# Optimization experiments

Hardware: AMD Instinct MI355X
Metric: run time of the kernel (lower is better)

Reference implementation:

```python
import jax, jax.numpy as jnp
import numpy as np

E, TOPK, D, F, FS = 16, 4, 2560, 1664, 3328
B, S = 1, 2048


def setup_inputs() -> dict:
    key = jax.random.key(0)
    ks = jax.random.split(key, 8)
    sc = lambda *sh: 1.0 / np.sqrt(sh[-2] if len(sh) > 1 else 1.0)
    return {
        "hidden_states": jax.random.normal(ks[0], (B, S, D), jnp.float32),
        "router_weight": jax.random.normal(ks[1], (E, D), jnp.float32) * (1.0 / np.sqrt(D)),
        "w_gate": jax.random.normal(ks[2], (E, D, F), jnp.float32) * (1.0 / np.sqrt(D)),
        "w_up": jax.random.normal(ks[3], (E, D, F), jnp.float32) * (1.0 / np.sqrt(D)),
        "w_down": jax.random.normal(ks[4], (E, F, D), jnp.float32) * (1.0 / np.sqrt(F)),
        "sw_gate": jax.random.normal(ks[5], (D, FS), jnp.float32) * (1.0 / np.sqrt(D)),
        "sw_up": jax.random.normal(ks[6], (D, FS), jnp.float32) * (1.0 / np.sqrt(D)),
        "sw_down": jax.random.normal(ks[7], (FS, D), jnp.float32) * (1.0 / np.sqrt(FS)),
    }


def reference(hidden_states, router_weight, w_gate, w_up, w_down, sw_gate, sw_up, sw_down):
    b, s, d = hidden_states.shape
    x = hidden_states.reshape(-1, d)  # [T, D]
    T = x.shape[0]

    # Router: linear -> softmax -> top-k -> renormalize (vLLM FusedMoE default)
    logits = x @ router_weight.T                      # [T, E]
    probs = jax.nn.softmax(logits, axis=-1)
    topk_w, topk_idx = jax.lax.top_k(probs, TOPK)     # [T, K]
    topk_w = topk_w / jnp.sum(topk_w, axis=-1, keepdims=True)
    combine = jnp.zeros((T, E), x.dtype).at[jnp.arange(T)[:, None], topk_idx].add(topk_w)  # [T, E]

    # Expert SiLU-gated MLPs (dense-dispatch reference for grouped GEMM)
    g = jnp.einsum('td,edf->tef', x, w_gate)          # [T, E, F]
    u = jnp.einsum('td,edf->tef', x, w_up)
    h = jax.nn.silu(g) * u
    y = jnp.einsum('tef,efd->ted', h, w_down)         # [T, E, D]
    sparse_out = jnp.einsum('ted,te->td', y, combine)

    # Shared expert: LlamaMLP with silu gate, no bias
    shared_out = (jax.nn.silu(x @ sw_gate) * (x @ sw_up)) @ sw_down

    return (sparse_out + shared_out).reshape(b, s, d)
```

## Files before the change

### kernel.cpp

```cpp
#include <hip/hip_runtime.h>
#include <hip/hip_bf16.h>
#include <stdint.h>

#define E_N 16
#define TOPK 4
#define DD 2560
#define FF 1664
#define FSS 3328
#define TT 2048

#define BK 32

typedef __attribute__((ext_vector_type(8))) __bf16 bf16x8;
typedef __attribute__((ext_vector_type(4))) float f32x4;

__device__ __forceinline__ unsigned short f2bf(float f) {
  return __builtin_bit_cast(unsigned short, (__bf16)f);
}
__device__ __forceinline__ unsigned int pk2(float a, float b) {
  return (unsigned int)f2bf(a) | ((unsigned int)f2bf(b) << 16);
}

#define GLOAD16(g, l)                                                          \
  __builtin_amdgcn_global_load_lds(                                            \
      (const __attribute__((address_space(1))) void*)(g),                      \
      (__attribute__((address_space(3))) void*)(l), 16, 0, 0)

#define SBAR() __builtin_amdgcn_s_barrier()
#define SCHED0() __builtin_amdgcn_sched_barrier(0)
#define VMW(N) asm volatile("s_waitcnt vmcnt(" #N ")" ::: "memory")

__device__ __forceinline__ void swz_block(int& bm, int& bn, int& bz) {
  int gx = gridDim.x, gy = gridDim.y;
  int nwg = gx * gy * gridDim.z;
  int flat = blockIdx.x + gx * (blockIdx.y + gy * blockIdx.z);
  if ((nwg & 7) == 0) flat = (flat & 7) * (nwg >> 3) + (flat >> 3);
  bm = flat % gx;
  int rest = flat / gx;
  bn = rest % gy;
  bz = rest / gy;
}

__global__ __launch_bounds__(256) void cvt_bf16_kernel(const float* __restrict__ in,
                                                       unsigned short* __restrict__ out) {
  size_t i = ((size_t)blockIdx.x * 256 + threadIdx.x) * 4;
  float4 v = *reinterpret_cast<const float4*>(in + i);
  ushort4 o;
  o.x = f2bf(v.x); o.y = f2bf(v.y); o.z = f2bf(v.z); o.w = f2bf(v.w);
  *reinterpret_cast<ushort4*>(out + i) = o;
}

__global__ __launch_bounds__(256) void tcvt_kernel(const float* __restrict__ in,
                                                   unsigned short* __restrict__ out,
                                                   int K, int N) {
  __shared__ float lds[64 * 65];
  int z = blockIdx.z;
  in += (size_t)z * K * N;
  out += (size_t)z * K * N;
  int k0 = blockIdx.x * 64, n0 = blockIdx.y * 64;
  int t = threadIdx.x;
#pragma unroll
  for (int j = 0; j < 4; ++j) {
    int idx = j * 256 + t;
    int r = idx >> 4, c = (idx & 15) * 4;
    float4 v = *reinterpret_cast<const float4*>(in + (size_t)(k0 + r) * N + n0 + c);
    lds[r * 65 + c] = v.x;
    lds[r * 65 + c + 1] = v.y;
    lds[r * 65 + c + 2] = v.z;
    lds[r * 65 + c + 3] = v.w;
  }
  __syncthreads();
#pragma unroll
  for (int j = 0; j < 2; ++j) {
    int idx = j * 256 + t;
    int n = idx >> 3, kg = (idx & 7) * 8;
    float a0 = lds[(kg + 0) * 65 + n], a1 = lds[(kg + 1) * 65 + n];
    float a2 = lds[(kg + 2) * 65 + n], a3 = lds[(kg + 3) * 65 + n];
    float a4 = lds[(kg + 4) * 65 + n], a5 = lds[(kg + 5) * 65 + n];
    float a6 = lds[(kg + 6) * 65 + n], a7 = lds[(kg + 7) * 65 + n];
    uint4 o{pk2(a0, a1), pk2(a2, a3), pk2(a4, a5), pk2(a6, a7)};
    *reinterpret_cast<uint4*>(out + (size_t)(n0 + n) * K + k0 + kg) = o;
  }
}

__global__ __launch_bounds__(256) void router_kernel(const float* __restrict__ x,
                                                     const float* __restrict__ rw,
                                                     int* __restrict__ cnt,
                                                     int* __restrict__ list,
                                                     float* __restrict__ tw) {
  int t = blockIdx.x;
  const float* xr = x + (size_t)t * DD;
  __shared__ float logits[E_N];
  int lane = threadIdx.x & 63, wid = threadIdx.x >> 6;
  for (int ee = 0; ee < 4; ++ee) {
    int e = wid * 4 + ee;
    const float* wr = rw + (size_t)e * DD;
    float p = 0.f;
    for (int d = lane; d < DD; d += 64) p += xr[d] * wr[d];
#pragma unroll
    for (int off = 32; off > 0; off >>= 1) p += __shfl_down(p, off);
    if (lane == 0) logits[e] = p;
  }
  __syncthreads();
  if (threadIdx.x == 0) {
    float mx = -1e30f;
    for (int e = 0; e < E_N; ++e) mx = fmaxf(mx, logits[e]);
    float pe[E_N];
    for (int e = 0; e < E_N; ++e) pe[e] = __expf(logits[e] - mx);
    int idx[TOPK]; float val[TOPK]; float s4 = 0.f;
    unsigned used = 0;
    for (int k = 0; k < TOPK; ++k) {
      int bi = 0; float bv = -1.f;
      for (int e = 0; e < E_N; ++e)
        if (!((used >> e) & 1) && pe[e] > bv) { bv = pe[e]; bi = e; }
      used |= 1u << bi; idx[k] = bi; val[k] = bv; s4 += bv;
    }
    float inv = 1.f / s4;
    for (int k = 0; k < TOPK; ++k) {
      int e2 = idx[k];
      int pos = atomicAdd(&cnt[e2], 1);
      list[e2 * TT + pos] = t * 4 + k;
      tw[t * 4 + k] = val[k] * inv;
    }
  }
}

__global__ __launch_bounds__(512, 2) void gu_kernel(
    const unsigned short* __restrict__ Xb,
    const unsigned short* __restrict__ WgT,
    const unsigned short* __restrict__ WuT,
    unsigned short* __restrict__ H,
    const int* __restrict__ list, const int* __restrict__ cnt,
    int Ktot, int Ntot, int Mfixed) {
  int bm, bn, e;
  swz_block(bm, bn, e);
  int M = cnt ? cnt[e] : Mfixed;
  int m0 = bm * 256;
  if (m0 >= M) return;
  int n0 = bn * 128;
  const unsigned short* Bg0 = WgT + (size_t)e * Ktot * Ntot;
  const unsigned short* Bu0 = WuT + (size_t)e * Ktot * Ntot;
  const int* lst = list ? (list + e * TT) : nullptr;

  __shared__ __align__(16) unsigned short lds[4][16384];

  int tid = threadIdx.x, lane = tid & 63, w = tid >> 6;
  int wm = w >> 1, wn = w & 1;

  const unsigned short* sp[4];
  {
    int rh = tid >> 2, c = tid & 3;
    int cs = (c ^ ((rh >> 1) & 3)) * 8;
    int a0 = min(m0 + rh, M - 1), a1 = min(m0 + 128 + rh, M - 1);
    int t0 = lst ? (lst[a0] >> 2) : a0;
    int t1 = lst ? (lst[a1] >> 2) : a1;
    sp[0] = Xb + (size_t)t0 * Ktot + cs;
    sp[1] = Xb + (size_t)t1 * Ktot + cs;
    sp[2] = Bg0 + (size_t)(n0 + rh) * Ktot + cs;
    sp[3] = Bu0 + (size_t)(n0 + rh) * Ktot + cs;
  }

  auto issue = [&](int kt, int buf) {
    int koff = kt * BK;
    unsigned short* d = &lds[buf][0];
#pragma unroll
    for (int j = 0; j < 4; ++j)
      GLOAD16(sp[j] + koff, d + j * 4096 + tid * 8);
  };

  int cg = lane >> 4;
  int aoff[4], goff[4];
#pragma unroll
  for (int mf = 0; mf < 4; ++mf) {
    int r = wm * 64 + mf * 16 + (lane & 15);
    aoff[mf] = r * 32 + ((cg ^ ((r >> 1) & 3)) * 8);
  }
#pragma unroll
  for (int nf = 0; nf < 4; ++nf) {
    int rb = wn * 64 + nf * 16 + (lane & 15);
    goff[nf] = 8192 + rb * 32 + ((cg ^ ((rb >> 1) & 3)) * 8);
  }

  f32x4 accG[4][4] = {};
  f32x4 accU[4][4] = {};

  auto compute = [&](int buf) {
    const unsigned short* L = &lds[buf][0];
    bf16x8 a[4], g[4], u[4];
#pragma unroll
    for (int mf = 0; mf < 4; ++mf)
      a[mf] = __builtin_bit_cast(bf16x8, *reinterpret_cast<const uint4*>(L + aoff[mf]));
#pragma unroll
    for (int nf = 0; nf < 4; ++nf) {
      g[nf] = __builtin_bit_cast(bf16x8, *reinterpret_cast<const uint4*>(L + goff[nf]));
      u[nf] = __builtin_bit_cast(bf16x8, *reinterpret_cast<const uint4*>(L + goff[nf] + 4096));
    }
    __builtin_amdgcn_s_setprio(1);
#pragma unroll
    for (int mf = 0; mf < 4; ++mf)
#pragma unroll
      for (int nf = 0; nf < 4; ++nf) {
        accG[mf][nf] = __builtin_amdgcn_mfma_f32_16x16x32_bf16(a[mf], g[nf], accG[mf][nf], 0, 0, 0);
        accU[mf][nf] = __builtin_amdgcn_mfma_f32_16x16x32_bf16(a[mf], u[nf], accU[mf][nf], 0, 0, 0);
      }
    __builtin_amdgcn_s_setprio(0);
  };

  int nk = Ktot / BK;
  issue(0, 0);
  issue(1, 1);
  issue(2, 2);
  for (int kt = 0; kt < nk; ++kt) {
    int rem = nk - 1 - kt;
    if (rem >= 3) { issue(kt + 3, (kt + 3) & 3); VMW(12); }
    else if (rem == 2) { VMW(8); }
    else if (rem == 1) { VMW(4); }
    else { VMW(0); }
    SCHED0();
    SBAR(); SCHED0();
    compute(kt & 3);
    SCHED0();
    SBAR(); SCHED0();
  }

#pragma unroll
  for (int mf = 0; mf < 4; ++mf) {
#pragma unroll
    for (int q = 0; q < 4; ++q) {
      int lr = wm * 64 + mf * 16 + (lane >> 4) * 4 + q;
      int grow = m0 + lr;
      if (grow < M) {
        int code = lst ? lst[grow] : grow;
        unsigned short* Hp = H + (size_t)code * Ntot + n0 + wn * 64 + (lane & 15);
#pragma unroll
        for (int nf = 0; nf < 4; ++nf) {
          float gg = accG[mf][nf][q], uu = accU[mf][nf][q];
          Hp[nf * 16] = f2bf((gg / (1.f + __expf(-gg))) * uu);
        }
      }
    }
  }
}

__global__ __launch_bounds__(512, 2) void dn_kernel(
    const unsigned short* __restrict__ Hb,
    const unsigned short* __restrict__ WT,
    float* __restrict__ Y,
    const int* __restrict__ list, const int* __restrict__ cnt,
    const float* __restrict__ tw, int Ktot, int Ntot, int Mfixed) {
  int bm, bn, e;
  swz_block(bm, bn, e);
  int M = cnt ? cnt[e] : Mfixed;
  int m0 = bm * 128;
  if (m0 >= M) return;
  int n0 = bn * 256;
  const unsigned short* B0 = WT + (size_t)e * Ktot * Ntot;
  const int* lst = list ? (list + e * TT) : nullptr;

  __shared__ __align__(16) unsigned short lds[4][12288];

  int tid = threadIdx.x, lane = tid & 63, w = tid >> 6;
  int wm = w >> 2, wn = w & 3;

  const unsigned short* sp[3];
  {
    int rh = tid >> 2, c = tid & 3;
    int cs = (c ^ ((rh >> 1) & 3)) * 8;
    int a0 = min(m0 + rh, M - 1);
    int code0 = lst ? lst[a0] : a0;
    sp[0] = Hb + (size_t)code0 * Ktot + cs;
    sp[1] = B0 + (size_t)(n0 + rh) * Ktot + cs;
    sp[2] = B0 + (size_t)(n0 + 128 + rh) * Ktot + cs;
  }

  auto issue = [&](int kt, int buf) {
    int koff = kt * BK;
    unsigned short* d = &lds[buf][0];
#pragma unroll
    for (int j = 0; j < 3; ++j)
      GLOAD16(sp[j] + koff, d + j * 4096 + tid * 8);
  };

  int cg = lane >> 4;
  int aoff[4], boff[4];
#pragma unroll
  for (int mf = 0; mf < 4; ++mf) {
    int r = wm * 64 + mf * 16 + (lane & 15);
    aoff[mf] = r * 32 + ((cg ^ ((r >> 1) & 3)) * 8);
  }
#pragma unroll
  for (int nf = 0; nf < 4; ++nf) {
    int rb = wn * 64 + nf * 16 + (lane & 15);
    boff[nf] = 4096 + rb * 32 + ((cg ^ ((rb >> 1) & 3)) * 8);
  }

  f32x4 acc[4][4] = {};

  auto compute = [&](int buf) {
    const unsigned short* L = &lds[buf][0];
    bf16x8 a[4], b[4];
#pragma unroll
    for (int mf = 0; mf < 4; ++mf)
      a[mf] = __builtin_bit_cast(bf16x8, *reinterpret_cast<const uint4*>(L + aoff[mf]));
#pragma unroll
    for (int nf = 0; nf < 4; ++nf)
      b[nf] = __builtin_bit_cast(bf16x8, *reinterpret_cast<const uint4*>(L + boff[nf]));
    __builtin_amdgcn_s_setprio(1);
#pragma unroll
    for (int mf = 0; mf < 4; ++mf)
#pragma unroll
      for (int nf = 0; nf < 4; ++nf)
        acc[mf][nf] = __builtin_amdgcn_mfma_f32_16x16x32_bf16(a[mf], b[nf], acc[mf][nf], 0, 0, 0);
    __builtin_amdgcn_s_setprio(0);
  };

  int nk = Ktot / BK;
  issue(0, 0);
  issue(1, 1);
  issue(2, 2);
  for (int kt = 0; kt < nk; ++kt) {
    int rem = nk - 1 - kt;
    if (rem >= 3) { issue(kt + 3, (kt + 3) & 3); VMW(9); }
    else if (rem == 2) { VMW(6); }
    else if (rem == 1) { VMW(3); }
    else { VMW(0); }
    SCHED0();
    SBAR(); SCHED0();
    compute(kt & 3);
    SCHED0();
    SBAR(); SCHED0();
  }

#pragma unroll
  for (int mf = 0; mf < 4; ++mf) {
#pragma unroll
    for (int q = 0; q < 4; ++q) {
      int lr = wm * 64 + mf * 16 + (lane >> 4) * 4 + q;
      int grow = m0 + lr;
      if (grow < M) {
        int code = lst ? lst[grow] : grow;
        float scale = tw ? tw[code] : 1.f;
        float* Yp = Y + (size_t)code * Ntot + n0 + wn * 64 + (lane & 15);
#pragma unroll
        for (int nf = 0; nf < 4; ++nf) Yp[nf * 16] = acc[mf][nf][q] * scale;
      }
    }
  }
}

__global__ __launch_bounds__(256) void combine_kernel(const float* __restrict__ Y,
                                                      const float* __restrict__ Ys,
                                                      float* __restrict__ out) {
  size_t i = ((size_t)blockIdx.x * 256 + threadIdx.x) * 4;
  size_t t = i / DD;
  int d = (int)(i % DD);
  float4 a = *reinterpret_cast<const float4*>(Ys + i);
#pragma unroll
  for (int k = 0; k < 4; ++k) {
    float4 v = *reinterpret_cast<const float4*>(Y + (t * 4 + k) * (size_t)DD + d);
    a.x += v.x; a.y += v.y; a.z += v.z; a.w += v.w;
  }
  *reinterpret_cast<float4*>(out + i) = a;
}

extern "C" void kernel_launch(void* const* d_in, const int* in_sizes, int n_in,
                              void* d_out, int out_size, void* d_ws, size_t ws_size,
                              hipStream_t stream) {
  const float* x  = (const float*)d_in[0];
  const float* rw = (const float*)d_in[1];
  const float* wg = (const float*)d_in[2];
  const float* wu = (const float*)d_in[3];
  const float* wd = (const float*)d_in[4];
  const float* sg = (const float*)d_in[5];
  const float* su = (const float*)d_in[6];
  const float* sd = (const float*)d_in[7];
  float* out = (float*)d_out;

  char* ws = (char*)d_ws;
  size_t off = 0;
  auto alloc = [&](size_t bytes) {
    off = (off + 255) & ~(size_t)255;
    void* p = ws + off;
    off += bytes;
    return p;
  };
  unsigned short* W1 = (unsigned short*)alloc((size_t)E_N * FF * DD * 2);
  unsigned short* W2 = (unsigned short*)alloc((size_t)E_N * FF * DD * 2);
  unsigned short* W3 = (unsigned short*)alloc((size_t)FSS * DD * 2);
  unsigned short* W4 = (unsigned short*)alloc((size_t)FSS * DD * 2);
  unsigned short* Xb = (unsigned short*)alloc((size_t)TT * DD * 2);
  unsigned short* Hx = (unsigned short*)alloc((size_t)4 * TT * FF * 2);
  unsigned short* Hs = (unsigned short*)alloc((size_t)TT * FSS * 2);
  float* Y  = (float*)alloc((size_t)4 * TT * DD * 4);
  float* Ys = (float*)alloc((size_t)TT * DD * 4);
  float* tw = (float*)alloc((size_t)4 * TT * 4);
  int* cnt  = (int*)alloc(E_N * 4);
  int* list = (int*)alloc((size_t)E_N * TT * 4);
  (void)ws_size; (void)in_sizes; (void)n_in; (void)out_size;

  hipMemsetAsync(cnt, 0, E_N * 4, stream);
  cvt_bf16_kernel<<<TT * DD / 4 / 256, 256, 0, stream>>>(x, Xb);
  router_kernel<<<TT, 256, 0, stream>>>(x, rw, cnt, list, tw);

  tcvt_kernel<<<dim3(DD / 64, FF / 64, E_N), 256, 0, stream>>>(wg, W1, DD, FF);
  tcvt_kernel<<<dim3(DD / 64, FF / 64, E_N), 256, 0, stream>>>(wu, W2, DD, FF);
  tcvt_kernel<<<dim3(DD / 64, FSS / 64, 1), 256, 0, stream>>>(sg, W3, DD, FSS);
  tcvt_kernel<<<dim3(DD / 64, FSS / 64, 1), 256, 0, stream>>>(su, W4, DD, FSS);

  gu_kernel<<<dim3(TT * 4 / 256, FF / 128, E_N), 512, 0, stream>>>(
      Xb, W1, W2, Hx, list, cnt, DD, FF, 0);
  gu_kernel<<<dim3(TT / 256, FSS / 128, 1), 512, 0, stream>>>(
      Xb, W3, W4, Hs, nullptr, nullptr, DD, FSS, TT);

  tcvt_kernel<<<dim3(FF / 64, DD / 64, E_N), 256, 0, stream>>>(wd, W1, FF, DD);
  tcvt_kernel<<<dim3(FSS / 64, DD / 64, 1), 256, 0, stream>>>(sd, W2, FSS, DD);

  dn_kernel<<<dim3(TT * 4 / 128, DD / 256, E_N), 512, 0, stream>>>(
      Hx, W1, Y, list, cnt, tw, FF, DD, 0);
  dn_kernel<<<dim3(TT / 128, DD / 256, 1), 512, 0, stream>>>(
      Hs, W2, Ys, nullptr, nullptr, nullptr, FSS, DD, TT);

  combine_kernel<<<TT * DD / 4 / 256, 256, 0, stream>>>(Y, Ys, out);
}
```

Baseline: 1.159 ms.

## Fuse fp32 weight transpose-convert into grouped GEMM B-tile loads

Removes the separate transpose-and-convert kernels that wrote bf16 copies of every expert and shared weight. The GEMM kernels now read fp32 weights straight from global memory into registers, pack them to bf16 and store them transposed into swizzled LDS. They double-buffer A through global-to-LDS loads and B through registers. Tiles shrink to 128x128 with 256 threads, which raises occupancy but doubles fp32 weight traffic per byte used and reloads weights once for each M tile.

```diff
diff --git a/kernel.cpp b/kernel.cpp
--- a/kernel.cpp
+++ b/kernel.cpp
@@ -9,8 +9,6 @@
 #define FSS 3328
 #define TT 2048
 
-#define BK 32
-
 typedef __attribute__((ext_vector_type(8))) __bf16 bf16x8;
 typedef __attribute__((ext_vector_type(4))) float f32x4;
 
@@ -29,6 +27,7 @@
 #define SBAR() __builtin_amdgcn_s_barrier()
 #define SCHED0() __builtin_amdgcn_sched_barrier(0)
 #define VMW(N) asm volatile("s_waitcnt vmcnt(" #N ")" ::: "memory")
+#define LGKM0() asm volatile("s_waitcnt lgkmcnt(0)" ::: "memory")
 
 __device__ __forceinline__ void swz_block(int& bm, int& bn, int& bz) {
   int gx = gridDim.x, gy = gridDim.y;
@@ -48,39 +47,6 @@
   ushort4 o;
   o.x = f2bf(v.x); o.y = f2bf(v.y); o.z = f2bf(v.z); o.w = f2bf(v.w);
   *reinterpret_cast<ushort4*>(out + i) = o;
-}
-
-__global__ __launch_bounds__(256) void tcvt_kernel(const float* __restrict__ in,
-                                                   unsigned short* __restrict__ out,
-                                                   int K, int N) {
-  __shared__ float lds[64 * 65];
-  int z = blockIdx.z;
-  in += (size_t)z * K * N;
-  out += (size_t)z * K * N;
-  int k0 = blockIdx.x * 64, n0 = blockIdx.y * 64;
-  int t = threadIdx.x;
-#pragma unroll
-  for (int j = 0; j < 4; ++j) {
-    int idx = j * 256 + t;
-    int r = idx >> 4, c = (idx & 15) * 4;
-    float4 v = *reinterpret_cast<const float4*>(in + (size_t)(k0 + r) * N + n0 + c);
-    lds[r * 65 + c] = v.x;
-    lds[r * 65 + c + 1] = v.y;
-    lds[r * 65 + c + 2] = v.z;
-    lds[r * 65 + c + 3] = v.w;
-  }
-  __syncthreads();
-#pragma unroll
-  for (int j = 0; j < 2; ++j) {
-    int idx = j * 256 + t;
-    int n = idx >> 3, kg = (idx & 7) * 8;
-    float a0 = lds[(kg + 0) * 65 + n], a1 = lds[(kg + 1) * 65 + n];
-    float a2 = lds[(kg + 2) * 65 + n], a3 = lds[(kg + 3) * 65 + n];
-    float a4 = lds[(kg + 4) * 65 + n], a5 = lds[(kg + 5) * 65 + n];
-    float a6 = lds[(kg + 6) * 65 + n], a7 = lds[(kg + 7) * 65 + n];
-    uint4 o{pk2(a0, a1), pk2(a2, a3), pk2(a4, a5), pk2(a6, a7)};
-    *reinterpret_cast<uint4*>(out + (size_t)(n0 + n) * K + k0 + kg) = o;
-  }
 }
 
 __global__ __launch_bounds__(256) void router_kernel(const float* __restrict__ x,
@@ -125,51 +91,52 @@
   }
 }
 
-__global__ __launch_bounds__(512, 2) void gu_kernel(
+__global__ __launch_bounds__(256, 2) void gu_kernel(
     const unsigned short* __restrict__ Xb,
-    const unsigned short* __restrict__ WgT,
-    const unsigned short* __restrict__ WuT,
+    const float* __restrict__ Wg,
+    const float* __restrict__ Wu,
     unsigned short* __restrict__ H,
     const int* __restrict__ list, const int* __restrict__ cnt,
     int Ktot, int Ntot, int Mfixed) {
   int bm, bn, e;
   swz_block(bm, bn, e);
   int M = cnt ? cnt[e] : Mfixed;
-  int m0 = bm * 256;
+  int m0 = bm * 128;
   if (m0 >= M) return;
   int n0 = bn * 128;
-  const unsigned short* Bg0 = WgT + (size_t)e * Ktot * Ntot;
-  const unsigned short* Bu0 = WuT + (size_t)e * Ktot * Ntot;
+  const float* G0 = Wg + (size_t)e * Ktot * Ntot;
+  const float* U0 = Wu + (size_t)e * Ktot * Ntot;
   const int* lst = list ? (list + e * TT) : nullptr;
 
-  __shared__ __align__(16) unsigned short lds[4][16384];
+  __shared__ __align__(16) unsigned short sA[2][4096];
+  __shared__ __align__(16) unsigned short sG[2][4096];
+  __shared__ __align__(16) unsigned short sU[2][4096];
 
   int tid = threadIdx.x, lane = tid & 63, w = tid >> 6;
-  int wm = w >> 1, wn = w & 1;
-
-  const unsigned short* sp[4];
-  {
-    int rh = tid >> 2, c = tid & 3;
-    int cs = (c ^ ((rh >> 1) & 3)) * 8;
-    int a0 = min(m0 + rh, M - 1), a1 = min(m0 + 128 + rh, M - 1);
-    int t0 = lst ? (lst[a0] >> 2) : a0;
-    int t1 = lst ? (lst[a1] >> 2) : a1;
-    sp[0] = Xb + (size_t)t0 * Ktot + cs;
-    sp[1] = Xb + (size_t)t1 * Ktot + cs;
-    sp[2] = Bg0 + (size_t)(n0 + rh) * Ktot + cs;
-    sp[3] = Bu0 + (size_t)(n0 + rh) * Ktot + cs;
-  }
-
-  auto issue = [&](int kt, int buf) {
-    int koff = kt * BK;
-    unsigned short* d = &lds[buf][0];
-#pragma unroll
-    for (int j = 0; j < 4; ++j)
-      GLOAD16(sp[j] + koff, d + j * 4096 + tid * 8);
-  };
-
-  int cg = lane >> 4;
-  int aoff[4], goff[4];
+
+  const unsigned short* pA[2];
+#pragma unroll
+  for (int q = 0; q < 2; ++q) {
+    int row = q * 64 + (tid >> 2);
+    int cs = (tid & 3) ^ ((row >> 1) & 3);
+    int ar = min(m0 + row, M - 1);
+    int tok = lst ? (lst[ar] >> 2) : ar;
+    pA[q] = Xb + (size_t)tok * Ktot + cs * 8;
+  }
+
+  int kq = tid >> 5, nq = tid & 31;
+  const float* pG = G0 + (size_t)(kq * 4) * Ntot + n0 + nq * 4;
+  const float* pU = U0 + (size_t)(kq * 4) * Ntot + n0 + nq * 4;
+
+  int wB[4];
+#pragma unroll
+  for (int i = 0; i < 4; ++i) {
+    int r = nq * 4 + i;
+    wB[i] = r * 32 + (((kq >> 1) ^ ((r >> 1) & 3)) * 8) + ((kq & 1) * 4);
+  }
+
+  int wm = w >> 1, wn = w & 1, cg = lane >> 4;
+  int aoff[4], boff[4];
 #pragma unroll
   for (int mf = 0; mf < 4; ++mf) {
     int r = wm * 64 + mf * 16 + (lane & 15);
@@ -178,22 +145,42 @@
 #pragma unroll
   for (int nf = 0; nf < 4; ++nf) {
     int rb = wn * 64 + nf * 16 + (lane & 15);
-    goff[nf] = 8192 + rb * 32 + ((cg ^ ((rb >> 1) & 3)) * 8);
+    boff[nf] = rb * 32 + ((cg ^ ((rb >> 1) & 3)) * 8);
   }
 
   f32x4 accG[4][4] = {};
   f32x4 accU[4][4] = {};
-
-  auto compute = [&](int buf) {
-    const unsigned short* L = &lds[buf][0];
+  float4 rG[4], rU[4];
+
+  auto issueA = [&](int kt, int b) {
+    GLOAD16(pA[0] + kt * 32, &sA[b][tid * 8]);
+    GLOAD16(pA[1] + kt * 32, &sA[b][2048 + tid * 8]);
+  };
+  auto issueB = [&](int kt) {
+#pragma unroll
+    for (int j = 0; j < 4; ++j) {
+      rG[j] = *reinterpret_cast<const float4*>(pG + (size_t)(kt * 32 + j) * Ntot);
+      rU[j] = *reinterpret_cast<const float4*>(pU + (size_t)(kt * 32 + j) * Ntot);
+    }
+  };
+  auto writeB = [&](int b) {
+#pragma unroll
+    for (int i = 0; i < 4; ++i) {
+      uint2 vg{pk2(rG[0][i], rG[1][i]), pk2(rG[2][i], rG[3][i])};
+      uint2 vu{pk2(rU[0][i], rU[1][i]), pk2(rU[2][i], rU[3][i])};
+      *reinterpret_cast<uint2*>(&sG[b][wB[i]]) = vg;
+      *reinterpret_cast<uint2*>(&sU[b][wB[i]]) = vu;
+    }
+  };
+  auto compute = [&](int b) {
     bf16x8 a[4], g[4], u[4];
 #pragma unroll
     for (int mf = 0; mf < 4; ++mf)
-      a[mf] = __builtin_bit_cast(bf16x8, *reinterpret_cast<const uint4*>(L + aoff[mf]));
+      a[mf] = __builtin_bit_cast(bf16x8, *reinterpret_cast<const uint4*>(&sA[b][aoff[mf]]));
 #pragma unroll
     for (int nf = 0; nf < 4; ++nf) {
-      g[nf] = __builtin_bit_cast(bf16x8, *reinterpret_cast<const uint4*>(L + goff[nf]));
-      u[nf] = __builtin_bit_cast(bf16x8, *reinterpret_cast<const uint4*>(L + goff[nf] + 4096));
+      g[nf] = __builtin_bit_cast(bf16x8, *reinterpret_cast<const uint4*>(&sG[b][boff[nf]]));
+      u[nf] = __builtin_bit_cast(bf16x8, *reinterpret_cast<const uint4*>(&sU[b][boff[nf]]));
     }
     __builtin_amdgcn_s_setprio(1);
 #pragma unroll
@@ -206,21 +193,26 @@
     __builtin_amdgcn_s_setprio(0);
   };
 
-  int nk = Ktot / BK;
-  issue(0, 0);
-  issue(1, 1);
-  issue(2, 2);
+  int nk = Ktot / 32;
+  issueB(0);
+  SCHED0();
+  issueA(0, 0);
+  issueA(1, 1);
+  SCHED0();
   for (int kt = 0; kt < nk; ++kt) {
-    int rem = nk - 1 - kt;
-    if (rem >= 3) { issue(kt + 3, (kt + 3) & 3); VMW(12); }
-    else if (rem == 2) { VMW(8); }
-    else if (rem == 1) { VMW(4); }
-    else { VMW(0); }
+    int b = kt & 1;
+    if (kt == nk - 1) { VMW(0); } else { VMW(2); }
+    SCHED0();
+    writeB(b);
+    if (kt + 1 < nk) issueB(kt + 1);
+    SCHED0();
+    LGKM0();
     SCHED0();
     SBAR(); SCHED0();
-    compute(kt & 3);
+    compute(b);
     SCHED0();
     SBAR(); SCHED0();
+    if (kt + 2 < nk) { issueA(kt + 2, b); SCHED0(); }
   }
 
 #pragma unroll
@@ -242,9 +234,9 @@
   }
 }
 
-__global__ __launch_bounds__(512, 2) void dn_kernel(
+__global__ __launch_bounds__(256, 3) void dn_kernel(
     const unsigned short* __restrict__ Hb,
-    const unsigned short* __restrict__ WT,
+    const float* __restrict__ Wd,
     float* __restrict__ Y,
     const int* __restrict__ list, const int* __restrict__ cnt,
     const float* __restrict__ tw, int Ktot, int Ntot, int Mfixed) {
@@ -253,35 +245,36 @@
   int M = cnt ? cnt[e] : Mfixed;
   int m0 = bm * 128;
   if (m0 >= M) return;
-  int n0 = bn * 256;
-  const unsigned short* B0 = WT + (size_t)e * Ktot * Ntot;
+  int n0 = bn * 128;
+  const float* B0 = Wd + (size_t)e * Ktot * Ntot;
   const int* lst = list ? (list + e * TT) : nullptr;
 
-  __shared__ __align__(16) unsigned short lds[4][12288];
+  __shared__ __align__(16) unsigned short sA[2][4096];
+  __shared__ __align__(16) unsigned short sB[2][4096];
 
   int tid = threadIdx.x, lane = tid & 63, w = tid >> 6;
-  int wm = w >> 2, wn = w & 3;
-
-  const unsigned short* sp[3];
-  {
-    int rh = tid >> 2, c = tid & 3;
-    int cs = (c ^ ((rh >> 1) & 3)) * 8;
-    int a0 = min(m0 + rh, M - 1);
-    int code0 = lst ? lst[a0] : a0;
-    sp[0] = Hb + (size_t)code0 * Ktot + cs;
-    sp[1] = B0 + (size_t)(n0 + rh) * Ktot + cs;
-    sp[2] = B0 + (size_t)(n0 + 128 + rh) * Ktot + cs;
-  }
-
-  auto issue = [&](int kt, int buf) {
-    int koff = kt * BK;
-    unsigned short* d = &lds[buf][0];
-#pragma unroll
-    for (int j = 0; j < 3; ++j)
-      GLOAD16(sp[j] + koff, d + j * 4096 + tid * 8);
-  };
-
-  int cg = lane >> 4;
+
+  const unsigned short* pA[2];
+#pragma unroll
+  for (int q = 0; q < 2; ++q) {
+    int row = q * 64 + (tid >> 2);
+    int cs = (tid & 3) ^ ((row >> 1) & 3);
+    int ar = min(m0 + row, M - 1);
+    int code = lst ? lst[ar] : ar;
+    pA[q] = Hb + (size_t)code * Ktot + cs * 8;
+  }
+
+  int kq = tid >> 5, nq = tid & 31;
+  const float* pB = B0 + (size_t)(kq * 4) * Ntot + n0 + nq * 4;
+
+  int wB[4];
+#pragma unroll
+  for (int i = 0; i < 4; ++i) {
+    int r = nq * 4 + i;
+    wB[i] = r * 32 + (((kq >> 1) ^ ((r >> 1) & 3)) * 8) + ((kq & 1) * 4);
+  }
+
+  int wm = w >> 1, wn = w & 1, cg = lane >> 4;
   int aoff[4], boff[4];
 #pragma unroll
   for (int mf = 0; mf < 4; ++mf) {
@@ -291,44 +284,65 @@
 #pragma unroll
   for (int nf = 0; nf < 4; ++nf) {
     int rb = wn * 64 + nf * 16 + (lane & 15);
-    boff[nf] = 4096 + rb * 32 + ((cg ^ ((rb >> 1) & 3)) * 8);
+    boff[nf] = rb * 32 + ((cg ^ ((rb >> 1) & 3)) * 8);
   }
 
   f32x4 acc[4][4] = {};
-
-  auto compute = [&](int buf) {
-    const unsigned short* L = &lds[buf][0];
-    bf16x8 a[4], b[4];
+  float4 rB[4];
+
+  auto issueA = [&](int kt, int b) {
+    GLOAD16(pA[0] + kt * 32, &sA[b][tid * 8]);
+    GLOAD16(pA[1] + kt * 32, &sA[b][2048 + tid * 8]);
+  };
+  auto issueB = [&](int kt) {
+#pragma unroll
+    for (int j = 0; j < 4; ++j)
+      rB[j] = *reinterpret_cast<const float4*>(pB + (size_t)(kt * 32 + j) * Ntot);
+  };
+  auto writeB = [&](int b) {
+#pragma unroll
+    for (int i = 0; i < 4; ++i) {
+      uint2 vb{pk2(rB[0][i], rB[1][i]), pk2(rB[2][i], rB[3][i])};
+      *reinterpret_cast<uint2*>(&sB[b][wB[i]]) = vb;
+    }
+  };
+  auto compute = [&](int b) {
+    bf16x8 a[4], bb[4];
 #pragma unroll
     for (int mf = 0; mf < 4; ++mf)
-      a[mf] = __builtin_bit_cast(bf16x8, *reinterpret_cast<const uint4*>(L + aoff[mf]));
+      a[mf] = __builtin_bit_cast(bf16x8, *reinterpret_cast<const uint4*>(&sA[b][aoff[mf]]));
 #pragma unroll
     for (int nf = 0; nf < 4; ++nf)
-      b[nf] = __builtin_bit_cast(bf16x8, *reinterpret_cast<const uint4*>(L + boff[nf]));
+      bb[nf] = __builtin_bit_cast(bf16x8, *reinterpret_cast<const uint4*>(&sB[b][boff[nf]]));
     __builtin_amdgcn_s_setprio(1);
 #pragma unroll
     for (int mf = 0; mf < 4; ++mf)
 #pragma unroll
       for (int nf = 0; nf < 4; ++nf)
-        acc[mf][nf] = __builtin_amdgcn_mfma_f32_16x16x32_bf16(a[mf], b[nf], acc[mf][nf], 0, 0, 0);
+        acc[mf][nf] = __builtin_amdgcn_mfma_f32_16x16x32_bf16(a[mf], bb[nf], acc[mf][nf], 0, 0, 0);
     __builtin_amdgcn_s_setprio(0);
   };
 
-  int nk = Ktot / BK;
-  issue(0, 0);
-  issue(1, 1);
-  issue(2, 2);
+  int nk = Ktot / 32;
+  issueB(0);
+  SCHED0();
+  issueA(0, 0);
+  issueA(1, 1);
+  SCHED0();
   for (int kt = 0; kt < nk; ++kt) {
-    int rem = nk - 1 - kt;
-    if (rem >= 3) { issue(kt + 3, (kt + 3) & 3); VMW(9); }
-    else if (rem == 2) { VMW(6); }
-    else if (rem == 1) { VMW(3); }
-    else { VMW(0); }
+    int b = kt & 1;
+    if (kt == nk - 1) { VMW(0); } else { VMW(2); }
+    SCHED0();
+    writeB(b);
+    if (kt + 1 < nk) issueB(kt + 1);
+    SCHED0();
+    LGKM0();
     SCHED0();
     SBAR(); SCHED0();
-    compute(kt & 3);
+    compute(b);
     SCHED0();
     SBAR(); SCHED0();
+    if (kt + 2 < nk) { issueA(kt + 2, b); SCHED0(); }
   }
 
 #pragma unroll
@@ -384,10 +398,6 @@
     off += bytes;
     return p;
   };
-  unsigned short* W1 = (unsigned short*)alloc((size_t)E_N * FF * DD * 2);
-  unsigned short* W2 = (unsigned short*)alloc((size_t)E_N * FF * DD * 2);
-  unsigned short* W3 = (unsigned short*)alloc((size_t)FSS * DD * 2);
-  unsigned short* W4 = (unsigned short*)alloc((size_t)FSS * DD * 2);
   unsigned short* Xb = (unsigned short*)alloc((size_t)TT * DD * 2);
   unsigned short* Hx = (unsigned short*)alloc((size_t)4 * TT * FF * 2);
   unsigned short* Hs = (unsigned short*)alloc((size_t)TT * FSS * 2);
@@ -402,23 +412,14 @@
   cvt_bf16_kernel<<<TT * DD / 4 / 256, 256, 0, stream>>>(x, Xb);
   router_kernel<<<TT, 256, 0, stream>>>(x, rw, cnt, list, tw);
 
-  tcvt_kernel<<<dim3(DD / 64, FF / 64, E_N), 256, 0, stream>>>(wg, W1, DD, FF);
-  tcvt_kernel<<<dim3(DD / 64, FF / 64, E_N), 256, 0, stream>>>(wu, W2, DD, FF);
-  tcvt_kernel<<<dim3(DD / 64, FSS / 64, 1), 256, 0, stream>>>(sg, W3, DD, FSS);
-  tcvt_kernel<<<dim3(DD / 64, FSS / 64, 1), 256, 0, stream>>>(su, W4, DD, FSS);
-
-  gu_kernel<<<dim3(TT * 4 / 256, FF / 128, E_N), 512, 0, stream>>>(
-      Xb, W1, W2, Hx, list, cnt, DD, FF, 0);
-  gu_kernel<<<dim3(TT / 256, FSS / 128, 1), 512, 0, stream>>>(
-      Xb, W3, W4, Hs, nullptr, nullptr, DD, FSS, TT);
-
-  tcvt_kernel<<<dim3(FF / 64, DD / 64, E_N), 256, 0, stream>>>(wd, W1, FF, DD);
-  tcvt_kernel<<<dim3(FSS / 64, DD / 64, 1), 256, 0, stream>>>(sd, W2, FSS, DD);
-
-  dn_kernel<<<dim3(TT * 4 / 128, DD / 256, E_N), 512, 0, stream>>>(
-      Hx, W1, Y, list, cnt, tw, FF, DD, 0);
-  dn_kernel<<<dim3(TT / 128, DD / 256, 1), 512, 0, stream>>>(
-      Hs, W2, Ys, nullptr, nullptr, nullptr, FSS, DD, TT);
+  gu_kernel<<<dim3(TT * 4 / 128, FF / 128, E_N), 256, 0, stream>>>(
+      Xb, wg, wu, Hx, list, cnt, DD, FF, 0);
+  gu_kernel<<<dim3(TT / 128, FSS / 128, 1), 256, 0, stream>>>(
+      Xb, sg, su, Hs, nullptr, nullptr, DD, FSS, TT);
+  dn_kernel<<<dim3(TT * 4 / 128, DD / 128, E_N), 256, 0, stream>>>(
+      Hx, wd, Y, list, cnt, tw, FF, DD, 0);
+  dn_kernel<<<dim3(TT / 128, DD / 128, 1), 256, 0, stream>>>(
+      Hs, sd, Ys, nullptr, nullptr, nullptr, FSS, DD, TT);
 
   combine_kernel<<<TT * DD / 4 / 256, 256, 0, stream>>>(Y, Ys, out);
 }
```

New measurement: 1.184 ms. +2.2%, slower.

## Unify GEMMs into one 256x256-tile kernel and split SiLU into a separate pass

Applied to the files above, without the earlier changes.

Replaces the fused gate/up kernel and the down-projection kernel with one templated 256x256-tile bf16 MFMA GEMM. It drops the trailing barrier by issuing the next prefetch after the leading barrier into the buffer freed in the previous iteration. Gate and up projections now run as separate GEMMs writing bf16 intermediates, and a new elementwise kernel applies SiLU(g)*u in place. The larger down-projection tile and the single barrier are meant to improve reuse and cut sync cost. In exchange it adds an extra launch and a global write and read of the gate intermediate, plus padded, bounds-checked tiles because FF is not a multiple of 256.

```diff
diff --git a/kernel.cpp b/kernel.cpp
--- a/kernel.cpp
+++ b/kernel.cpp
@@ -16,6 +16,9 @@
 
 __device__ __forceinline__ unsigned short f2bf(float f) {
   return __builtin_bit_cast(unsigned short, (__bf16)f);
+}
+__device__ __forceinline__ float bf2f(unsigned short u) {
+  return __builtin_bit_cast(float, (unsigned int)u << 16);
 }
 __device__ __forceinline__ unsigned int pk2(float a, float b) {
   return (unsigned int)f2bf(a) | ((unsigned int)f2bf(b) << 16);
@@ -125,84 +128,84 @@
   }
 }
 
-__global__ __launch_bounds__(512, 2) void gu_kernel(
-    const unsigned short* __restrict__ Xb,
-    const unsigned short* __restrict__ WgT,
-    const unsigned short* __restrict__ WuT,
-    unsigned short* __restrict__ H,
+template <int MODE>
+__global__ __launch_bounds__(512, 2) void g1_kernel(
+    const unsigned short* __restrict__ Ab,
+    const unsigned short* __restrict__ WT,
+    void* __restrict__ Out,
     const int* __restrict__ list, const int* __restrict__ cnt,
+    const float* __restrict__ tw,
     int Ktot, int Ntot, int Mfixed) {
   int bm, bn, e;
   swz_block(bm, bn, e);
   int M = cnt ? cnt[e] : Mfixed;
   int m0 = bm * 256;
   if (m0 >= M) return;
-  int n0 = bn * 128;
-  const unsigned short* Bg0 = WgT + (size_t)e * Ktot * Ntot;
-  const unsigned short* Bu0 = WuT + (size_t)e * Ktot * Ntot;
+  int n0 = bn * 256;
+  const unsigned short* B0 = WT + (size_t)e * Ktot * Ntot;
   const int* lst = list ? (list + e * TT) : nullptr;
 
   __shared__ __align__(16) unsigned short lds[4][16384];
 
   int tid = threadIdx.x, lane = tid & 63, w = tid >> 6;
-  int wm = w >> 1, wn = w & 1;
-
-  const unsigned short* sp[4];
-  {
-    int rh = tid >> 2, c = tid & 3;
-    int cs = (c ^ ((rh >> 1) & 3)) * 8;
-    int a0 = min(m0 + rh, M - 1), a1 = min(m0 + 128 + rh, M - 1);
-    int t0 = lst ? (lst[a0] >> 2) : a0;
-    int t1 = lst ? (lst[a1] >> 2) : a1;
-    sp[0] = Xb + (size_t)t0 * Ktot + cs;
-    sp[1] = Xb + (size_t)t1 * Ktot + cs;
-    sp[2] = Bg0 + (size_t)(n0 + rh) * Ktot + cs;
-    sp[3] = Bu0 + (size_t)(n0 + rh) * Ktot + cs;
+  int wm = w >> 2, wn = w & 3;
+
+  const unsigned short* pA[2];
+  const unsigned short* pB[2];
+#pragma unroll
+  for (int j = 0; j < 2; ++j) {
+    int idx = j * 512 + tid;
+    int row = idx >> 2, c = idx & 3;
+    int cs = c ^ ((row >> 1) & 3);
+    int ar = min(m0 + row, M - 1);
+    int code = lst ? lst[ar] : ar;
+    int arow = (MODE == 0) ? (lst ? (code >> 2) : code) : code;
+    pA[j] = Ab + (size_t)arow * Ktot + cs * 8;
+    int br = min(n0 + row, Ntot - 1);
+    pB[j] = B0 + (size_t)br * Ktot + cs * 8;
   }
 
   auto issue = [&](int kt, int buf) {
     int koff = kt * BK;
     unsigned short* d = &lds[buf][0];
 #pragma unroll
-    for (int j = 0; j < 4; ++j)
-      GLOAD16(sp[j] + koff, d + j * 4096 + tid * 8);
+    for (int j = 0; j < 2; ++j)
+      GLOAD16(pA[j] + koff, d + (j * 512 + tid) * 8);
+#pragma unroll
+    for (int j = 0; j < 2; ++j)
+      GLOAD16(pB[j] + koff, d + 8192 + (j * 512 + tid) * 8);
   };
 
   int cg = lane >> 4;
-  int aoff[4], goff[4];
-#pragma unroll
-  for (int mf = 0; mf < 4; ++mf) {
-    int r = wm * 64 + mf * 16 + (lane & 15);
+  int aoff[8], boff[4];
+#pragma unroll
+  for (int mf = 0; mf < 8; ++mf) {
+    int r = wm * 128 + mf * 16 + (lane & 15);
     aoff[mf] = r * 32 + ((cg ^ ((r >> 1) & 3)) * 8);
   }
 #pragma unroll
   for (int nf = 0; nf < 4; ++nf) {
     int rb = wn * 64 + nf * 16 + (lane & 15);
-    goff[nf] = 8192 + rb * 32 + ((cg ^ ((rb >> 1) & 3)) * 8);
-  }
-
-  f32x4 accG[4][4] = {};
-  f32x4 accU[4][4] = {};
+    boff[nf] = 8192 + rb * 32 + ((cg ^ ((rb >> 1) & 3)) * 8);
+  }
+
+  f32x4 acc[8][4] = {};
 
   auto compute = [&](int buf) {
     const unsigned short* L = &lds[buf][0];
-    bf16x8 a[4], g[4], u[4];
-#pragma unroll
-    for (int mf = 0; mf < 4; ++mf)
+    bf16x8 a[8], b[4];
+#pragma unroll
+    for (int mf = 0; mf < 8; ++mf)
       a[mf] = __builtin_bit_cast(bf16x8, *reinterpret_cast<const uint4*>(L + aoff[mf]));
 #pragma unroll
-    for (int nf = 0; nf < 4; ++nf) {
-      g[nf] = __builtin_bit_cast(bf16x8, *reinterpret_cast<const uint4*>(L + goff[nf]));
-      u[nf] = __builtin_bit_cast(bf16x8, *reinterpret_cast<const uint4*>(L + goff[nf] + 4096));
-    }
+    for (int nf = 0; nf < 4; ++nf)
+      b[nf] = __builtin_bit_cast(bf16x8, *reinterpret_cast<const uint4*>(L + boff[nf]));
     __builtin_amdgcn_s_setprio(1);
 #pragma unroll
-    for (int mf = 0; mf < 4; ++mf)
-#pragma unroll
-      for (int nf = 0; nf < 4; ++nf) {
-        accG[mf][nf] = __builtin_amdgcn_mfma_f32_16x16x32_bf16(a[mf], g[nf], accG[mf][nf], 0, 0, 0);
-        accU[mf][nf] = __builtin_amdgcn_mfma_f32_16x16x32_bf16(a[mf], u[nf], accU[mf][nf], 0, 0, 0);
-      }
+    for (int mf = 0; mf < 8; ++mf)
+#pragma unroll
+      for (int nf = 0; nf < 4; ++nf)
+        acc[mf][nf] = __builtin_amdgcn_mfma_f32_16x16x32_bf16(a[mf], b[nf], acc[mf][nf], 0, 0, 0);
     __builtin_amdgcn_s_setprio(0);
   };
 
@@ -212,140 +215,62 @@
   issue(2, 2);
   for (int kt = 0; kt < nk; ++kt) {
     int rem = nk - 1 - kt;
-    if (rem >= 3) { issue(kt + 3, (kt + 3) & 3); VMW(12); }
-    else if (rem == 2) { VMW(8); }
+    if (rem >= 2) { VMW(8); }
     else if (rem == 1) { VMW(4); }
     else { VMW(0); }
     SCHED0();
     SBAR(); SCHED0();
+    if (rem >= 3) { issue(kt + 3, (kt + 3) & 3); SCHED0(); }
     compute(kt & 3);
     SCHED0();
-    SBAR(); SCHED0();
-  }
-
-#pragma unroll
-  for (int mf = 0; mf < 4; ++mf) {
+  }
+
+#pragma unroll
+  for (int mf = 0; mf < 8; ++mf) {
 #pragma unroll
     for (int q = 0; q < 4; ++q) {
-      int lr = wm * 64 + mf * 16 + (lane >> 4) * 4 + q;
+      int lr = wm * 128 + mf * 16 + (lane >> 4) * 4 + q;
       int grow = m0 + lr;
       if (grow < M) {
         int code = lst ? lst[grow] : grow;
-        unsigned short* Hp = H + (size_t)code * Ntot + n0 + wn * 64 + (lane & 15);
-#pragma unroll
-        for (int nf = 0; nf < 4; ++nf) {
-          float gg = accG[mf][nf][q], uu = accU[mf][nf][q];
-          Hp[nf * 16] = f2bf((gg / (1.f + __expf(-gg))) * uu);
+        int colb = n0 + wn * 64 + (lane & 15);
+        if (MODE == 0) {
+          unsigned short* Op = (unsigned short*)Out + (size_t)code * Ntot + colb;
+#pragma unroll
+          for (int nf = 0; nf < 4; ++nf)
+            if (colb + nf * 16 < Ntot) Op[nf * 16] = f2bf(acc[mf][nf][q]);
+        } else {
+          float scale = tw ? tw[code] : 1.f;
+          float* Op = (float*)Out + (size_t)code * Ntot + colb;
+#pragma unroll
+          for (int nf = 0; nf < 4; ++nf)
+            if (colb + nf * 16 < Ntot) Op[nf * 16] = acc[mf][nf][q] * scale;
         }
       }
     }
   }
 }
 
-__global__ __launch_bounds__(512, 2) void dn_kernel(
-    const unsigned short* __restrict__ Hb,
-    const unsigned short* __restrict__ WT,
-    float* __restrict__ Y,
-    const int* __restrict__ list, const int* __restrict__ cnt,
-    const float* __restrict__ tw, int Ktot, int Ntot, int Mfixed) {
-  int bm, bn, e;
-  swz_block(bm, bn, e);
-  int M = cnt ? cnt[e] : Mfixed;
-  int m0 = bm * 128;
-  if (m0 >= M) return;
-  int n0 = bn * 256;
-  const unsigned short* B0 = WT + (size_t)e * Ktot * Ntot;
-  const int* lst = list ? (list + e * TT) : nullptr;
-
-  __shared__ __align__(16) unsigned short lds[4][12288];
-
-  int tid = threadIdx.x, lane = tid & 63, w = tid >> 6;
-  int wm = w >> 2, wn = w & 3;
-
-  const unsigned short* sp[3];
-  {
-    int rh = tid >> 2, c = tid & 3;
-    int cs = (c ^ ((rh >> 1) & 3)) * 8;
-    int a0 = min(m0 + rh, M - 1);
-    int code0 = lst ? lst[a0] : a0;
-    sp[0] = Hb + (size_t)code0 * Ktot + cs;
-    sp[1] = B0 + (size_t)(n0 + rh) * Ktot + cs;
-    sp[2] = B0 + (size_t)(n0 + 128 + rh) * Ktot + cs;
-  }
-
-  auto issue = [&](int kt, int buf) {
-    int koff = kt * BK;
-    unsigned short* d = &lds[buf][0];
-#pragma unroll
-    for (int j = 0; j < 3; ++j)
-      GLOAD16(sp[j] + koff, d + j * 4096 + tid * 8);
-  };
-
-  int cg = lane >> 4;
-  int aoff[4], boff[4];
-#pragma unroll
-  for (int mf = 0; mf < 4; ++mf) {
-    int r = wm * 64 + mf * 16 + (lane & 15);
-    aoff[mf] = r * 32 + ((cg ^ ((r >> 1) & 3)) * 8);
-  }
-#pragma unroll
-  for (int nf = 0; nf < 4; ++nf) {
-    int rb = wn * 64 + nf * 16 + (lane & 15);
-    boff[nf] = 4096 + rb * 32 + ((cg ^ ((rb >> 1) & 3)) * 8);
-  }
-
-  f32x4 acc[4][4] = {};
-
-  auto compute = [&](int buf) {
-    const unsigned short* L = &lds[buf][0];
-    bf16x8 a[4], b[4];
-#pragma unroll
-    for (int mf = 0; mf < 4; ++mf)
-      a[mf] = __builtin_bit_cast(bf16x8, *reinterpret_cast<const uint4*>(L + aoff[mf]));
-#pragma unroll
-    for (int nf = 0; nf < 4; ++nf)
-      b[nf] = __builtin_bit_cast(bf16x8, *reinterpret_cast<const uint4*>(L + boff[nf]));
-    __builtin_amdgcn_s_setprio(1);
-#pragma unroll
-    for (int mf = 0; mf < 4; ++mf)
-#pragma unroll
-      for (int nf = 0; nf < 4; ++nf)
-        acc[mf][nf] = __builtin_amdgcn_mfma_f32_16x16x32_bf16(a[mf], b[nf], acc[mf][nf], 0, 0, 0);
-    __builtin_amdgcn_s_setprio(0);
-  };
-
-  int nk = Ktot / BK;
-  issue(0, 0);
-  issue(1, 1);
-  issue(2, 2);
-  for (int kt = 0; kt < nk; ++kt) {
-    int rem = nk - 1 - kt;
-    if (rem >= 3) { issue(kt + 3, (kt + 3) & 3); VMW(9); }
-    else if (rem == 2) { VMW(6); }
-    else if (rem == 1) { VMW(3); }
-    else { VMW(0); }
-    SCHED0();
-    SBAR(); SCHED0();
-    compute(kt & 3);
-    SCHED0();
-    SBAR(); SCHED0();
-  }
-
-#pragma unroll
-  for (int mf = 0; mf < 4; ++mf) {
-#pragma unroll
-    for (int q = 0; q < 4; ++q) {
-      int lr = wm * 64 + mf * 16 + (lane >> 4) * 4 + q;
-      int grow = m0 + lr;
-      if (grow < M) {
-        int code = lst ? lst[grow] : grow;
-        float scale = tw ? tw[code] : 1.f;
-        float* Yp = Y + (size_t)code * Ntot + n0 + wn * 64 + (lane & 15);
-#pragma unroll
-        for (int nf = 0; nf < 4; ++nf) Yp[nf * 16] = acc[mf][nf][q] * scale;
-      }
-    }
-  }
+__global__ __launch_bounds__(256) void h_kernel(const unsigned short* __restrict__ g,
+                                                unsigned short* __restrict__ u) {
+  size_t i = ((size_t)blockIdx.x * 256 + threadIdx.x) * 8;
+  uint4 gv = *reinterpret_cast<const uint4*>(g + i);
+  uint4 uv = *reinterpret_cast<const uint4*>(u + i);
+  const unsigned int* gw = reinterpret_cast<const unsigned int*>(&gv);
+  const unsigned int* uw = reinterpret_cast<const unsigned int*>(&uv);
+  uint4 ov;
+  unsigned int* ow = reinterpret_cast<unsigned int*>(&ov);
+#pragma unroll
+  for (int j = 0; j < 4; ++j) {
+    float g0 = bf2f((unsigned short)(gw[j] & 0xffff));
+    float g1 = bf2f((unsigned short)(gw[j] >> 16));
+    float u0 = bf2f((unsigned short)(uw[j] & 0xffff));
+    float u1 = bf2f((unsigned short)(uw[j] >> 16));
+    float h0 = (g0 / (1.f + __expf(-g0))) * u0;
+    float h1 = (g1 / (1.f + __expf(-g1))) * u1;
+    ow[j] = pk2(h0, h1);
+  }
+  *reinterpret_cast<uint4*>(u + i) = ov;
 }
 
 __global__ __launch_bounds__(256) void combine_kernel(const float* __restrict__ Y,
@@ -389,7 +314,9 @@
   unsigned short* W3 = (unsigned short*)alloc((size_t)FSS * DD * 2);
   unsigned short* W4 = (unsigned short*)alloc((size_t)FSS * DD * 2);
   unsigned short* Xb = (unsigned short*)alloc((size_t)TT * DD * 2);
+  unsigned short* Gx = (unsigned short*)alloc((size_t)4 * TT * FF * 2);
   unsigned short* Hx = (unsigned short*)alloc((size_t)4 * TT * FF * 2);
+  unsigned short* Gs = (unsigned short*)alloc((size_t)TT * FSS * 2);
   unsigned short* Hs = (unsigned short*)alloc((size_t)TT * FSS * 2);
   float* Y  = (float*)alloc((size_t)4 * TT * DD * 4);
   float* Ys = (float*)alloc((size_t)TT * DD * 4);
@@ -407,17 +334,24 @@
   tcvt_kernel<<<dim3(DD / 64, FSS / 64, 1), 256, 0, stream>>>(sg, W3, DD, FSS);
   tcvt_kernel<<<dim3(DD / 64, FSS / 64, 1), 256, 0, stream>>>(su, W4, DD, FSS);
 
-  gu_kernel<<<dim3(TT * 4 / 256, FF / 128, E_N), 512, 0, stream>>>(
-      Xb, W1, W2, Hx, list, cnt, DD, FF, 0);
-  gu_kernel<<<dim3(TT / 256, FSS / 128, 1), 512, 0, stream>>>(
-      Xb, W3, W4, Hs, nullptr, nullptr, DD, FSS, TT);
+  g1_kernel<0><<<dim3(TT * 4 / 256, (FF + 255) / 256, E_N), 512, 0, stream>>>(
+      Xb, W1, Gx, list, cnt, nullptr, DD, FF, 0);
+  g1_kernel<0><<<dim3(TT * 4 / 256, (FF + 255) / 256, E_N), 512, 0, stream>>>(
+      Xb, W2, Hx, list, cnt, nullptr, DD, FF, 0);
+  h_kernel<<<(size_t)4 * TT * FF / 8 / 256, 256, 0, stream>>>(Gx, Hx);
+
+  g1_kernel<0><<<dim3(TT / 256, FSS / 256, 1), 512, 0, stream>>>(
+      Xb, W3, Gs, nullptr, nullptr, nullptr, DD, FSS, TT);
+  g1_kernel<0><<<dim3(TT / 256, FSS / 256, 1), 512, 0, stream>>>(
+      Xb, W4, Hs, nullptr, nullptr, nullptr, DD, FSS, TT);
+  h_kernel<<<(size_t)TT * FSS / 8 / 256, 256, 0, stream>>>(Gs, Hs);
 
   tcvt_kernel<<<dim3(FF / 64, DD / 64, E_N), 256, 0, stream>>>(wd, W1, FF, DD);
   tcvt_kernel<<<dim3(FSS / 64, DD / 64, 1), 256, 0, stream>>>(sd, W2, FSS, DD);
 
-  dn_kernel<<<dim3(TT * 4 / 128, DD / 256, E_N), 512, 0, stream>>>(
+  g1_kernel<1><<<dim3(TT * 4 / 256, DD / 256, E_N), 512, 0, stream>>>(
       Hx, W1, Y, list, cnt, tw, FF, DD, 0);
-  dn_kernel<<<dim3(TT / 128, DD / 256, 1), 512, 0, stream>>>(
+  g1_kernel<1><<<dim3(TT / 256, DD / 256, 1), 512, 0, stream>>>(
       Hs, W2, Ys, nullptr, nullptr, nullptr, FSS, DD, TT);
 
   combine_kernel<<<TT * DD / 4 / 256, 256, 0, stream>>>(Y, Ys, out);
```

Result: slower. 1.268 ms (+9.4%).
